# Kernel tuning notes

Hardware: AMD Instinct MI355X
Metric: run time of the kernel (lower is better)

The kernel has to match this reference:

```python
import jax, jax.numpy as jnp
import numpy as np

UNITS = 1024
D_Q = 1024
D_V = 1024


def setup_inputs() -> dict:
    key = jax.random.key(0)
    ks = jax.random.split(key, 8)
    B, S = 32, 2048
    query = jax.random.normal(ks[0], (B, D_Q), dtype=jnp.float32)
    values = jax.random.normal(ks[1], (B, S, D_V), dtype=jnp.float32)
    # Keras Dense params (glorot-ish scale for weights, zero bias init kept random-free)
    W1 = jax.random.normal(ks[2], (D_V, UNITS), dtype=jnp.float32) / np.sqrt(D_V)
    b1 = jnp.zeros((UNITS,), dtype=jnp.float32)
    W2 = jax.random.normal(ks[3], (D_Q, UNITS), dtype=jnp.float32) / np.sqrt(D_Q)
    b2 = jnp.zeros((UNITS,), dtype=jnp.float32)
    V = jax.random.normal(ks[4], (UNITS, 1), dtype=jnp.float32) / np.sqrt(UNITS)
    bV = jnp.zeros((1,), dtype=jnp.float32)
    return {"query": query, "values": values, "W1": W1, "b1": b1,
            "W2": W2, "b2": b2, "V": V, "bV": bV}


def reference(query, values, W1, b1, W2, b2, V, bV):
    # query: [B, d_q], values: [B, S, d_v]
    proj_v = jnp.einsum('bsd,du->bsu', values, W1) + b1        # [B, S, U]
    proj_q = (query @ W2 + b2)[:, None, :]                      # [B, 1, U]
    score = jnp.tanh(proj_v + proj_q) @ V + bV                  # [B, S, 1]
    attention_weights = jax.nn.softmax(score, axis=1)           # [B, S, 1]
    context_vector = jnp.sum(attention_weights * values, axis=1)  # [B, d_v]
    return (context_vector, attention_weights)
```

## Files before the change

### kernel.cpp

```cpp
#include <hip/hip_runtime.h>
#include <math.h>

#define B_  32
#define S_  2048
#define DV  1024
#define U_  1024

typedef __attribute__((ext_vector_type(8))) short bf16x8;
typedef __attribute__((ext_vector_type(4))) float f32x4;

__device__ inline unsigned short f2bf(float f) {
    unsigned int x = __float_as_uint(f);
    return (unsigned short)((x + 0x7fffu + ((x >> 16) & 1u)) >> 16);
}

__device__ inline float tanh_fast(float x) {
    float ax = fabsf(x);
    float e  = __expf(ax + ax);
    float t  = 1.0f - __fdividef(2.0f, e + 1.0f);
    return copysignf(t, x);
}

__device__ __forceinline__ void gload16(const void* g, void* l) {
    __builtin_amdgcn_global_load_lds(
        (const __attribute__((address_space(1))) void*)g,
        (__attribute__((address_space(3))) void*)l,
        16, 0, 0);
}

#define ASM_VMCNT(N) asm volatile("s_waitcnt vmcnt(" #N ")" ::: "memory")
#define ASM_LGKM0()  do { asm volatile("s_waitcnt lgkmcnt(0)" ::: "memory"); \
                          __builtin_amdgcn_sched_barrier(0); } while (0)

__global__ void init_kernel(const float* __restrict__ b1, const float* __restrict__ b2,
                            float* __restrict__ t, float* __restrict__ ctx,
                            float* __restrict__ scores) {
    int i = blockIdx.x * 256 + threadIdx.x;
    scores[i] = 0.f;
    if (i < B_ * U_) {
        int u = i & (U_ - 1);
        t[i]   = b1[u] + b2[u];
        ctx[i] = 0.f;
    }
}

__global__ void projq_kernel(const float* __restrict__ q, const float* __restrict__ W2,
                             float* __restrict__ t) {
    int b  = blockIdx.x;
    int ks = blockIdx.y;
    int tid = threadIdx.x;
    __shared__ float qs[64];
    if (tid < 64) qs[tid] = q[b * DV + ks * 64 + tid];
    __syncthreads();
    float a0 = 0.f, a1 = 0.f, a2 = 0.f, a3 = 0.f;
    const float* w = W2 + (size_t)(ks * 64) * U_;
    for (int d = 0; d < 64; ++d) {
        float qd = qs[d];
        const float* wr = w + (size_t)d * U_ + tid;
        a0 += qd * wr[0];
        a1 += qd * wr[256];
        a2 += qd * wr[512];
        a3 += qd * wr[768];
    }
    atomicAdd(&t[b * U_ + tid      ], a0);
    atomicAdd(&t[b * U_ + tid + 256], a1);
    atomicAdd(&t[b * U_ + tid + 512], a2);
    atomicAdd(&t[b * U_ + tid + 768], a3);
}

__global__ void cvt_values_tiled(const float* __restrict__ v, char* __restrict__ o) {
    size_t t = (size_t)blockIdx.x * 256 + threadIdx.x;
    size_t i = t * 8;
    int row = (int)(i >> 10);
    int k   = (int)(i & 1023);
    float4 f0 = *(const float4*)(v + i);
    float4 f1 = *(const float4*)(v + i + 4);
    union { unsigned short s[8]; uint4 u; } p;
    p.s[0] = f2bf(f0.x); p.s[1] = f2bf(f0.y); p.s[2] = f2bf(f0.z); p.s[3] = f2bf(f0.w);
    p.s[4] = f2bf(f1.x); p.s[5] = f2bf(f1.y); p.s[6] = f2bf(f1.z); p.s[7] = f2bf(f1.w);
    int stile = row >> 8, rt = row & 255, h = rt >> 7, r = rt & 127;
    int kt = k >> 6, kk = k & 63;
    int pchunk = (kk >> 3) ^ (r & 7);
    size_t dst = (size_t)stile * 524288 + (size_t)kt * 32768
               + h * 16384 + r * 128 + pchunk * 16;
    *(uint4*)(o + dst) = p.u;
}

__global__ void prep_w1t(const float* __restrict__ W1, unsigned short* __restrict__ W1T) {
    __shared__ float tile[64][65];
    int k0 = blockIdx.x * 64, u0 = blockIdx.y * 64;
    int t = threadIdx.x;
    int lr = t >> 4, lc = (t & 15) * 4;
#pragma unroll
    for (int i = 0; i < 4; ++i) {
        float4 f = *(const float4*)&W1[(size_t)(k0 + lr + i * 16) * U_ + u0 + lc];
        tile[lr + i * 16][lc + 0] = f.x; tile[lr + i * 16][lc + 1] = f.y;
        tile[lr + i * 16][lc + 2] = f.z; tile[lr + i * 16][lc + 3] = f.w;
    }
    __syncthreads();
    int ur = t >> 2, kq = (t & 3) * 16;
    union { unsigned short s[8]; uint4 u; } p0, p1;
#pragma unroll
    for (int e = 0; e < 8; ++e) p0.s[e] = f2bf(tile[kq + e][ur]);
#pragma unroll
    for (int e = 0; e < 8; ++e) p1.s[e] = f2bf(tile[kq + 8 + e][ur]);
    unsigned short* dst = W1T + (size_t)(u0 + ur) * 1024 + k0 + kq;
    *(uint4*)dst       = p0.u;
    *(uint4*)(dst + 8) = p1.u;
}

#define MFMA16(MB, NB)                                                          \
    _Pragma("unroll") for (int ks = 0; ks < 2; ++ks)                            \
    _Pragma("unroll") for (int n = 0; n < 2; ++n)                               \
    _Pragma("unroll") for (int m = 0; m < 4; ++m)                               \
        acc[(MB)+m][(NB)+n] = __builtin_amdgcn_mfma_f32_16x16x32_bf16(          \
            af[m][ks], bf[n][ks], acc[(MB)+m][(NB)+n], 0, 0, 0);

__launch_bounds__(512, 2)
__global__ void scores_mfma8(const char* __restrict__ AbfT,
                             const unsigned short* __restrict__ W1T,
                             const float* __restrict__ tvec,
                             const float* __restrict__ V,
                             float* __restrict__ scores) {
    __shared__ __align__(16) char lds[131072];

    const int tid  = threadIdx.x;
    const int lane = tid & 63;
    const int wave = tid >> 6;
    const int wm   = wave >> 2;
    const int wn   = wave & 3;
    const int l15  = lane & 15;
    const int lq   = lane >> 4;

    const int id    = blockIdx.x;
    const int wg    = (id & 7) * 128 + (id >> 3);
    const int utile = wg & 3;
    const int stile = wg >> 2;
    const size_t row0 = (size_t)stile * 256;
    const int b       = (int)(row0 >> 11);
    const int s_local = (int)(row0 & 2047);
    const int u0      = utile * 256;

    const char* aBase = AbfT + (size_t)stile * 524288 + wave * 1024 + lane * 16;
    const int rowst = wave * 8 + (lane >> 3);
    const int kch8  = ((lane & 7) ^ ((lane >> 3) & 7)) * 8;
    const unsigned short* bSrc = W1T + (size_t)(u0 + rowst) * 1024 + kch8;
    char* const dstW = lds + wave * 1024;

    const int ao0 = wm * 16384 + l15 * 128 + ((lq ^ (l15 & 7)) << 4);
    const int ao1 = ao0 ^ 64;
    const int bo0 = 32768 + (wn >> 1) * 16384 + (wn & 1) * 8192
                  + l15 * 128 + ((lq ^ (l15 & 7)) << 4);
    const int bo1 = bo0 ^ 64;

    f32x4 acc[8][4];
#pragma unroll
    for (int m = 0; m < 8; ++m)
#pragma unroll
        for (int n = 0; n < 4; ++n) acc[m][n] = (f32x4)0.f;

    bf16x8 af[4][2];
    bf16x8 bf[2][2];

    auto stageA = [&](size_t gOff, int dOff) {
        gload16(aBase + gOff,        dstW + dOff);
        gload16(aBase + gOff + 8192, dstW + dOff + 8192);
    };
    auto stageB = [&](const unsigned short* s, int dOff) {
        gload16(s,             dstW + dOff);
        gload16(s + 64 * 1024, dstW + dOff + 8192);
    };
    auto readA4 = [&](int base) {
#pragma unroll
        for (int m = 0; m < 4; ++m) {
            af[m][0] = *(const bf16x8*)(lds + base + m * 2048 + ao0);
            af[m][1] = *(const bf16x8*)(lds + base + m * 2048 + ao1);
        }
    };
    auto readB2 = [&](int base) {
#pragma unroll
        for (int n = 0; n < 2; ++n) {
            bf[n][0] = *(const bf16x8*)(lds + base + n * 2048 + bo0);
            bf[n][1] = *(const bf16x8*)(lds + base + n * 2048 + bo1);
        }
    };

    stageA(0,     0);
    stageA(16384, 16384);
    stageB(bSrc,          32768);
    stageB(bSrc + 131072, 49152);
    stageA(32768, 65536);
    __builtin_amdgcn_sched_barrier(0);
    ASM_VMCNT(2);
    __builtin_amdgcn_s_barrier();
    __builtin_amdgcn_sched_barrier(0);

    for (int it = 0; it < 8; ++it) {
        const bool pf = (it < 7);
        const size_t aIt = (size_t)it * 65536;
        readA4(0);
        readB2(0);
        stageA(aIt + 49152, 81920);
        __builtin_amdgcn_s_barrier();
        ASM_LGKM0();
        __builtin_amdgcn_s_setprio(1);
        MFMA16(0, 0);
        __builtin_amdgcn_s_setprio(0);
        __builtin_amdgcn_s_barrier();
        readB2(2 * 2048);
        stageB(bSrc + 64, 98304);
        __builtin_amdgcn_s_barrier();
        ASM_LGKM0();
        __builtin_amdgcn_s_setprio(1);
        MFMA16(0, 2);
        __builtin_amdgcn_s_setprio(0);
        __builtin_amdgcn_s_barrier();
        readA4(4 * 2048);
        stageB(bSrc + 64 + 131072, 114688);
        __builtin_amdgcn_s_barrier();
        ASM_LGKM0();
        __builtin_amdgcn_s_setprio(1);
        MFMA16(4, 2);
        __builtin_amdgcn_s_setprio(0);
        __builtin_amdgcn_s_barrier();
        readB2(0);
        if (pf) stageA(aIt + 65536, 0);
        __builtin_amdgcn_s_barrier();
        ASM_LGKM0();
        __builtin_amdgcn_s_setprio(1);
        MFMA16(4, 0);
        __builtin_amdgcn_s_setprio(0);
        __builtin_amdgcn_sched_barrier(0);
        if (pf) { ASM_VMCNT(2); } else { ASM_VMCNT(0); }
        __builtin_amdgcn_s_barrier();
        __builtin_amdgcn_sched_barrier(0);
        readA4(65536);
        readB2(65536);
        if (pf) stageA(aIt + 81920, 16384);
        __builtin_amdgcn_s_barrier();
        ASM_LGKM0();
        __builtin_amdgcn_s_setprio(1);
        MFMA16(0, 0);
        __builtin_amdgcn_s_setprio(0);
        __builtin_amdgcn_s_barrier();
        readB2(65536 + 2 * 2048);
        if (pf) stageB(bSrc + 128, 32768);
        __builtin_amdgcn_s_barrier();
        ASM_LGKM0();
        __builtin_amdgcn_s_setprio(1);
        MFMA16(0, 2);
        __builtin_amdgcn_s_setprio(0);
        __builtin_amdgcn_s_barrier();
        readA4(65536 + 4 * 2048);
        if (pf) stageB(bSrc + 128 + 131072, 49152);
        __builtin_amdgcn_s_barrier();
        ASM_LGKM0();
        __builtin_amdgcn_s_setprio(1);
        MFMA16(4, 2);
        __builtin_amdgcn_s_setprio(0);
        __builtin_amdgcn_s_barrier();
        readB2(65536);
        if (pf) stageA(aIt + 98304, 65536);
        __builtin_amdgcn_s_barrier();
        ASM_LGKM0();
        __builtin_amdgcn_s_setprio(1);
        MFMA16(4, 0);
        __builtin_amdgcn_s_setprio(0);
        __builtin_amdgcn_sched_barrier(0);
        if (pf) { ASM_VMCNT(2); }
        __builtin_amdgcn_s_barrier();
        __builtin_amdgcn_sched_barrier(0);

        bSrc += 128;
    }

    __syncthreads();
    float* fscore = (float*)lds;
    if (tid < 256) fscore[tid] = 0.f;
    __syncthreads();
    float tu[4], vu[4];
#pragma unroll
    for (int n = 0; n < 4; ++n) {
        int u = u0 + wn * 64 + n * 16 + l15;
        tu[n] = tvec[b * U_ + u];
        vu[n] = V[u];
    }
#pragma unroll
    for (int m = 0; m < 8; ++m) {
#pragma unroll
        for (int r = 0; r < 4; ++r) {
            float p = 0.f;
#pragma unroll
            for (int n = 0; n < 4; ++n) p += tanh_fast(acc[m][n][r] + tu[n]) * vu[n];
            p += __shfl_xor(p, 1);
            p += __shfl_xor(p, 2);
            p += __shfl_xor(p, 4);
            p += __shfl_xor(p, 8);
            if (l15 == 0) atomicAdd(&fscore[wm * 128 + m * 16 + lq * 4 + r], p);
        }
    }
    __syncthreads();
    if (tid < 256) atomicAdd(&scores[(size_t)b * S_ + s_local + tid], fscore[tid]);
}

template<bool ABF16>
__launch_bounds__(256, 2)
__global__ void scores_mfma(const void* __restrict__ aPtr,
                            const unsigned short* __restrict__ W1T,
                            const float* __restrict__ t,
                            const float* __restrict__ V,
                            float* __restrict__ scores) {
    __shared__ unsigned short sA[128 * 40];
    __shared__ unsigned short sB[256 * 40];
    __shared__ float fscore[128];

    const int tid  = threadIdx.x;
    const int lane = tid & 63;
    const int wave = tid >> 6;
    const int wm = wave & 1, wn = wave >> 1;
    const int l15 = lane & 15, lq = lane >> 4;

    const int id    = blockIdx.x;
    const int utile = (id >> 3) & 3;
    const int stile = (id & 7) | ((id >> 5) << 3);
    const size_t row0 = (size_t)stile * 128;
    const int b       = (int)(row0 >> 11);
    const int s_local = (int)(row0 & 2047);
    const int u0      = utile * 256;

    if (tid < 128) fscore[tid] = 0.f;

    const int ar = tid >> 1, ak = (tid & 1) << 4;
    const int br = tid >> 1, bk = (tid & 1) << 4;

    const float* Af = (const float*)aPtr + (row0 + ar) * 1024 + ak;
    const unsigned short* Ab = (const unsigned short*)aPtr + (row0 + ar) * 1024 + ak;
    const unsigned short* Bp0 = W1T + (size_t)(u0 + br) * 1024 + bk;
    const unsigned short* Bp1 = Bp0 + 128 * 1024;

    f32x4 acc[4][8];
#pragma unroll
    for (int i = 0; i < 4; ++i)
#pragma unroll
        for (int j = 0; j < 8; ++j) acc[i][j] = (f32x4)0.f;

    uint4 sa0, sa1, sb0, sb1, sb2, sb3;
    float4 fa0, fa1, fa2, fa3;

    if (ABF16) {
        sa0 = *(const uint4*)(Ab);
        sa1 = *(const uint4*)(Ab + 8);
    } else {
        fa0 = *(const float4*)(Af);
        fa1 = *(const float4*)(Af + 4);
        fa2 = *(const float4*)(Af + 8);
        fa3 = *(const float4*)(Af + 12);
    }
    sb0 = *(const uint4*)(Bp0);
    sb1 = *(const uint4*)(Bp0 + 8);
    sb2 = *(const uint4*)(Bp1);
    sb3 = *(const uint4*)(Bp1 + 8);

    for (int k0 = 0; k0 < 1024; k0 += 32) {
        __syncthreads();
        if (ABF16) {
            *(uint4*)&sA[ar * 40 + ak]     = sa0;
            *(uint4*)&sA[ar * 40 + ak + 8] = sa1;
        } else {
            union { unsigned short s[8]; uint4 u; } p0, p1;
            p0.s[0] = f2bf(fa0.x); p0.s[1] = f2bf(fa0.y); p0.s[2] = f2bf(fa0.z); p0.s[3] = f2bf(fa0.w);
            p0.s[4] = f2bf(fa1.x); p0.s[5] = f2bf(fa1.y); p0.s[6] = f2bf(fa1.z); p0.s[7] = f2bf(fa1.w);
            p1.s[0] = f2bf(fa2.x); p1.s[1] = f2bf(fa2.y); p1.s[2] = f2bf(fa2.z); p1.s[3] = f2bf(fa2.w);
            p1.s[4] = f2bf(fa3.x); p1.s[5] = f2bf(fa3.y); p1.s[6] = f2bf(fa3.z); p1.s[7] = f2bf(fa3.w);
            *(uint4*)&sA[ar * 40 + ak]     = p0.u;
            *(uint4*)&sA[ar * 40 + ak + 8] = p1.u;
        }
        *(uint4*)&sB[br * 40 + bk]           = sb0;
        *(uint4*)&sB[br * 40 + bk + 8]       = sb1;
        *(uint4*)&sB[(br + 128) * 40 + bk]     = sb2;
        *(uint4*)&sB[(br + 128) * 40 + bk + 8] = sb3;

        if (k0 + 32 < 1024) {
            int nk = k0 + 32;
            if (ABF16) {
                sa0 = *(const uint4*)(Ab + nk);
                sa1 = *(const uint4*)(Ab + nk + 8);
            } else {
                fa0 = *(const float4*)(Af + nk);
                fa1 = *(const float4*)(Af + nk + 4);
                fa2 = *(const float4*)(Af + nk + 8);
                fa3 = *(const float4*)(Af + nk + 12);
            }
            sb0 = *(const uint4*)(Bp0 + nk);
            sb1 = *(const uint4*)(Bp0 + nk + 8);
            sb2 = *(const uint4*)(Bp1 + nk);
            sb3 = *(const uint4*)(Bp1 + nk + 8);
        }
        __syncthreads();

        bf16x8 af[4];
#pragma unroll
        for (int i = 0; i < 4; ++i)
            af[i] = *(const bf16x8*)&sA[(64 * wm + 16 * i + l15) * 40 + lq * 8];
#pragma unroll
        for (int j = 0; j < 8; ++j) {
            bf16x8 bfj = *(const bf16x8*)&sB[(128 * wn + 16 * j + l15) * 40 + lq * 8];
#pragma unroll
            for (int i = 0; i < 4; ++i)
                acc[i][j] = __builtin_amdgcn_mfma_f32_16x16x32_bf16(af[i], bfj, acc[i][j], 0, 0, 0);
        }
    }

    float tu[8], vu[8];
#pragma unroll
    for (int j = 0; j < 8; ++j) {
        int u = u0 + 128 * wn + 16 * j + l15;
        tu[j] = t[b * U_ + u];
        vu[j] = V[u];
    }
#pragma unroll
    for (int i = 0; i < 4; ++i) {
#pragma unroll
        for (int r = 0; r < 4; ++r) {
            float p = 0.f;
#pragma unroll
            for (int j = 0; j < 8; ++j) p += tanh_fast(acc[i][j][r] + tu[j]) * vu[j];
            p += __shfl_xor(p, 1);
            p += __shfl_xor(p, 2);
            p += __shfl_xor(p, 4);
            p += __shfl_xor(p, 8);
            if (l15 == 0) atomicAdd(&fscore[64 * wm + 16 * i + lq * 4 + r], p);
        }
    }
    __syncthreads();
    if (tid < 128) atomicAdd(&scores[(size_t)b * S_ + s_local + tid], fscore[tid]);
}

__launch_bounds__(256, 2)
__global__ void scores_vec(const float* __restrict__ values, const float* __restrict__ W1,
                           const float* __restrict__ t, const float* __restrict__ V,
                           float* __restrict__ scores) {
    __shared__ float vA[16][132];
    __shared__ float vB[16][68];
    __shared__ float fscore[128];
    const int b   = blockIdx.y;
    const int s0  = blockIdx.x * 128;
    const int tid = threadIdx.x;
    const int tx  = tid & 15, ty = tid >> 4;
    if (tid < 128) fscore[tid] = 0.f;
    const float* vbase = values + ((size_t)b * S_ + s0) * (size_t)DV;
    const int lm = tid >> 2, lkq = (tid & 3) * 4;
    const int lbk = tid >> 4, lbj = (tid & 15) * 4;
    for (int nt = 0; nt < U_ / 64; ++nt) {
        const int u0 = nt * 64;
        float acc[8][4];
#pragma unroll
        for (int i = 0; i < 8; ++i)
#pragma unroll
            for (int j = 0; j < 4; ++j) acc[i][j] = 0.f;
        for (int k0 = 0; k0 < DV; k0 += 16) {
            __syncthreads();
            const float4 v0 = *(const float4*)(vbase + (size_t)lm * DV + k0 + lkq);
            const float4 v1 = *(const float4*)(vbase + (size_t)(lm + 64) * DV + k0 + lkq);
            vA[lkq + 0][lm] = v0.x; vA[lkq + 1][lm] = v0.y;
            vA[lkq + 2][lm] = v0.z; vA[lkq + 3][lm] = v0.w;
            vA[lkq + 0][lm + 64] = v1.x; vA[lkq + 1][lm + 64] = v1.y;
            vA[lkq + 2][lm + 64] = v1.z; vA[lkq + 3][lm + 64] = v1.w;
            *(float4*)&vB[lbk][lbj] = *(const float4*)(W1 + (size_t)(k0 + lbk) * U_ + u0 + lbj);
            __syncthreads();
#pragma unroll
            for (int k = 0; k < 16; ++k) {
                float4 va0 = *(const float4*)&vA[k][ty * 8];
                float4 va1 = *(const float4*)&vA[k][ty * 8 + 4];
                float4 vb  = *(const float4*)&vB[k][tx * 4];
                float a_[8] = {va0.x, va0.y, va0.z, va0.w, va1.x, va1.y, va1.z, va1.w};
                float b_[4] = {vb.x, vb.y, vb.z, vb.w};
#pragma unroll
                for (int i = 0; i < 8; ++i)
#pragma unroll
                    for (int j = 0; j < 4; ++j) acc[i][j] += a_[i] * b_[j];
            }
        }
        float tq[4], vv[4];
#pragma unroll
        for (int j = 0; j < 4; ++j) {
            int u = u0 + tx * 4 + j;
            tq[j] = t[b * U_ + u];
            vv[j] = V[u];
        }
#pragma unroll
        for (int i = 0; i < 8; ++i) {
            float p = 0.f;
#pragma unroll
            for (int j = 0; j < 4; ++j) p += tanhf(acc[i][j] + tq[j]) * vv[j];
            p += __shfl_down(p, 8, 16);
            p += __shfl_down(p, 4, 16);
            p += __shfl_down(p, 2, 16);
            p += __shfl_down(p, 1, 16);
            if (tx == 0) fscore[ty * 8 + i] += p;
        }
    }
    __syncthreads();
    if (tid < 128) scores[(size_t)b * S_ + s0 + tid] = fscore[tid];
}

__global__ void softmax_kernel(const float* __restrict__ scores, float* __restrict__ wout) {
    int b = blockIdx.x;
    int tid = threadIdx.x;
    __shared__ float red[256];
    float v[8];
    float m = -1e30f;
#pragma unroll
    for (int i = 0; i < 8; ++i) {
        v[i] = scores[(size_t)b * S_ + tid + i * 256];
        m = fmaxf(m, v[i]);
    }
    red[tid] = m; __syncthreads();
    for (int off = 128; off > 0; off >>= 1) {
        if (tid < off) red[tid] = fmaxf(red[tid], red[tid + off]);
        __syncthreads();
    }
    m = red[0];
    __syncthreads();
    float s = 0.f;
#pragma unroll
    for (int i = 0; i < 8; ++i) { v[i] = __expf(v[i] - m); s += v[i]; }
    red[tid] = s; __syncthreads();
    for (int off = 128; off > 0; off >>= 1) {
        if (tid < off) red[tid] += red[tid + off];
        __syncthreads();
    }
    float inv = 1.f / red[0];
#pragma unroll
    for (int i = 0; i < 8; ++i) wout[(size_t)b * S_ + tid + i * 256] = v[i] * inv;
}

__global__ void context_kernel(const float* __restrict__ values, const float* __restrict__ w,
                               float* __restrict__ ctx) {
    int b   = blockIdx.x;
    int sc  = blockIdx.y;
    int tid = threadIdx.x;
    __shared__ float ws_[128];
    if (tid < 128) ws_[tid] = w[(size_t)b * S_ + sc * 128 + tid];
    __syncthreads();
    const float4* vp = (const float4*)(values + ((size_t)b * S_ + sc * 128) * DV) + tid;
    float ax = 0.f, ay = 0.f, az = 0.f, aw = 0.f;
#pragma unroll 4
    for (int s = 0; s < 128; ++s) {
        float4 v = vp[(size_t)s * 256];
        float wv = ws_[s];
        ax += wv * v.x; ay += wv * v.y; az += wv * v.z; aw += wv * v.w;
    }
    float* c = ctx + b * DV + tid * 4;
    atomicAdd(c + 0, ax); atomicAdd(c + 1, ay);
    atomicAdd(c + 2, az); atomicAdd(c + 3, aw);
}

extern "C" void kernel_launch(void* const* d_in, const int* in_sizes, int n_in,
                              void* d_out, int out_size, void* d_ws, size_t ws_size,
                              hipStream_t stream) {
    const float* query  = (const float*)d_in[0];
    const float* values = (const float*)d_in[1];
    const float* W1     = (const float*)d_in[2];
    const float* b1     = (const float*)d_in[3];
    const float* W2     = (const float*)d_in[4];
    const float* b2     = (const float*)d_in[5];
    const float* V      = (const float*)d_in[6];

    float* out  = (float*)d_out;
    float* ctx  = out;
    float* wout = out + B_ * DV;

    char* ws = (char*)d_ws;
    const size_t W1T_BYTES = (size_t)U_ * DV * 2;
    const size_t T_BYTES   = (size_t)B_ * U_ * 4;
    const size_t SC_BYTES  = (size_t)B_ * S_ * 4;
    const size_t ABF_BYTES = (size_t)B_ * S_ * DV * 2;

    if (ws_size >= W1T_BYTES + T_BYTES + SC_BYTES + ABF_BYTES) {
        unsigned short* W1T = (unsigned short*)ws;
        float* t      = (float*)(ws + W1T_BYTES);
        float* scores = t + B_ * U_;
        char*  AbfT   = (char*)(scores + B_ * S_);

        init_kernel     <<<dim3(256),      256, 0, stream>>>(b1, b2, t, ctx, scores);
        projq_kernel    <<<dim3(32, 16),   256, 0, stream>>>(query, W2, t);
        cvt_values_tiled<<<dim3(32768),    256, 0, stream>>>(values, AbfT);
        prep_w1t        <<<dim3(16, 16),   256, 0, stream>>>(W1, W1T);
        scores_mfma8    <<<dim3(1024),     512, 0, stream>>>(AbfT, W1T, t, V, scores);
        softmax_kernel  <<<dim3(32),       256, 0, stream>>>(scores, wout);
        context_kernel  <<<dim3(32, 16),   256, 0, stream>>>(values, wout, ctx);
    } else if (ws_size >= W1T_BYTES + T_BYTES + SC_BYTES) {
        unsigned short* W1T = (unsigned short*)ws;
        float* t      = (float*)(ws + W1T_BYTES);
        float* scores = t + B_ * U_;

        init_kernel   <<<dim3(256),      256, 0, stream>>>(b1, b2, t, ctx, scores);
        projq_kernel  <<<dim3(32, 16),   256, 0, stream>>>(query, W2, t);
        prep_w1t      <<<dim3(16, 16),   256, 0, stream>>>(W1, W1T);
        scores_mfma<false><<<dim3(2048), 256, 0, stream>>>(values, W1T, t, V, scores);
        softmax_kernel<<<dim3(32),       256, 0, stream>>>(scores, wout);
        context_kernel<<<dim3(32, 16),   256, 0, stream>>>(values, wout, ctx);
    } else {
        float* t      = (float*)ws;
        float* scores = t + B_ * U_;

        init_kernel   <<<dim3(256),      256, 0, stream>>>(b1, b2, t, ctx, scores);
        projq_kernel  <<<dim3(32, 16),   256, 0, stream>>>(query, W2, t);
        scores_vec    <<<dim3(16, 32),   256, 0, stream>>>(values, W1, t, V, scores);
        softmax_kernel<<<dim3(32),       256, 0, stream>>>(scores, wout);
        context_kernel<<<dim3(32, 16),   256, 0, stream>>>(values, wout, ctx);
    }
}
```

Measured before the change: 603.9 us.

## Fuse prep kernels into one launch and merge softmax with context

Merges init, query projection, values bf16 conversion and W1 transpose into a single heterogeneous kernel that picks its role from the block index. The query projection now has each block do a full-K dot product, so it writes the bias-plus-projection result directly without atomics. Softmax and the context reduction are fused into one kernel in which every block recomputes the row max and sum for its batch before weighting its 128-row slice. This cuts the launch count from seven to three and removes inter-kernel gaps, at the cost of redundant softmax reductions across the 16 slices of each batch row.

New measurement: 616.1 us. +2.0%, slower.

```diff
diff --git a/kernel.cpp b/kernel.cpp
--- a/kernel.cpp
+++ b/kernel.cpp
@@ -31,6 +31,330 @@
 #define ASM_VMCNT(N) asm volatile("s_waitcnt vmcnt(" #N ")" ::: "memory")
 #define ASM_LGKM0()  do { asm volatile("s_waitcnt lgkmcnt(0)" ::: "memory"); \
                           __builtin_amdgcn_sched_barrier(0); } while (0)
+
+__global__ __launch_bounds__(256)
+void fused_prep(const float* __restrict__ values, char* __restrict__ AbfT,
+                const float* __restrict__ W1, unsigned short* __restrict__ W1T,
+                const float* __restrict__ query, const float* __restrict__ W2,
+                const float* __restrict__ b1, const float* __restrict__ b2,
+                float* __restrict__ t, float* __restrict__ scores,
+                float* __restrict__ ctx) {
+    const int bid = blockIdx.x;
+    const int tid = threadIdx.x;
+
+    if (bid < 32768) {
+        size_t i = ((size_t)bid * 256 + tid) * 8;
+        int row = (int)(i >> 10);
+        int k   = (int)(i & 1023);
+        float4 f0 = *(const float4*)(values + i);
+        float4 f1 = *(const float4*)(values + i + 4);
+        union { unsigned short s[8]; uint4 u; } p;
+        p.s[0] = f2bf(f0.x); p.s[1] = f2bf(f0.y); p.s[2] = f2bf(f0.z); p.s[3] = f2bf(f0.w);
+        p.s[4] = f2bf(f1.x); p.s[5] = f2bf(f1.y); p.s[6] = f2bf(f1.z); p.s[7] = f2bf(f1.w);
+        int stile = row >> 8, rt = row & 255, h = rt >> 7, r = rt & 127;
+        int kt = k >> 6, kk = k & 63;
+        int pchunk = (kk >> 3) ^ (r & 7);
+        size_t dst = (size_t)stile * 524288 + (size_t)kt * 32768
+                   + h * 16384 + r * 128 + pchunk * 16;
+        *(uint4*)(AbfT + dst) = p.u;
+    } else if (bid < 33024) {
+        __shared__ float tile[64][65];
+        int i = bid - 32768;
+        int k0 = (i & 15) * 64, u0 = (i >> 4) * 64;
+        int lr = tid >> 4, lc = (tid & 15) * 4;
+#pragma unroll
+        for (int j = 0; j < 4; ++j) {
+            float4 f = *(const float4*)&W1[(size_t)(k0 + lr + j * 16) * U_ + u0 + lc];
+            tile[lr + j * 16][lc + 0] = f.x; tile[lr + j * 16][lc + 1] = f.y;
+            tile[lr + j * 16][lc + 2] = f.z; tile[lr + j * 16][lc + 3] = f.w;
+        }
+        __syncthreads();
+        int ur = tid >> 2, kq = (tid & 3) * 16;
+        union { unsigned short s[8]; uint4 u; } p0, p1;
+#pragma unroll
+        for (int e = 0; e < 8; ++e) p0.s[e] = f2bf(tile[kq + e][ur]);
+#pragma unroll
+        for (int e = 0; e < 8; ++e) p1.s[e] = f2bf(tile[kq + 8 + e][ur]);
+        unsigned short* dst = W1T + (size_t)(u0 + ur) * 1024 + k0 + kq;
+        *(uint4*)dst       = p0.u;
+        *(uint4*)(dst + 8) = p1.u;
+    } else if (bid < 33152) {
+        __shared__ float qs2[1024];
+        int i = bid - 33024;
+        int b = i >> 2, uq = i & 3;
+        for (int j = tid; j < 1024; j += 256) qs2[j] = query[b * DV + j];
+        __syncthreads();
+        int u = uq * 256 + tid;
+        float a0 = 0.f, a1 = 0.f, a2 = 0.f, a3 = 0.f;
+        float a4 = 0.f, a5 = 0.f, a6 = 0.f, a7 = 0.f;
+        const float* w = W2 + u;
+        for (int k = 0; k < 1024; k += 8) {
+            a0 += qs2[k + 0] * w[(size_t)(k + 0) * U_];
+            a1 += qs2[k + 1] * w[(size_t)(k + 1) * U_];
+            a2 += qs2[k + 2] * w[(size_t)(k + 2) * U_];
+            a3 += qs2[k + 3] * w[(size_t)(k + 3) * U_];
+            a4 += qs2[k + 4] * w[(size_t)(k + 4) * U_];
+            a5 += qs2[k + 5] * w[(size_t)(k + 5) * U_];
+            a6 += qs2[k + 6] * w[(size_t)(k + 6) * U_];
+            a7 += qs2[k + 7] * w[(size_t)(k + 7) * U_];
+        }
+        t[b * U_ + u] = b1[u] + b2[u]
+                      + ((a0 + a1) + (a2 + a3)) + ((a4 + a5) + (a6 + a7));
+    } else if (bid < 33408) {
+        scores[(bid - 33152) * 256 + tid] = 0.f;
+    } else {
+        ctx[(bid - 33408) * 256 + tid] = 0.f;
+    }
+}
+
+#define MFMA16(MB, NB)                                                          \
+    _Pragma("unroll") for (int ks = 0; ks < 2; ++ks)                            \
+    _Pragma("unroll") for (int n = 0; n < 2; ++n)                               \
+    _Pragma("unroll") for (int m = 0; m < 4; ++m)                               \
+        acc[(MB)+m][(NB)+n] = __builtin_amdgcn_mfma_f32_16x16x32_bf16(          \
+            af[m][ks], bf[n][ks], acc[(MB)+m][(NB)+n], 0, 0, 0);
+
+__launch_bounds__(512, 2)
+__global__ void scores_mfma8(const char* __restrict__ AbfT,
+                             const unsigned short* __restrict__ W1T,
+                             const float* __restrict__ tvec,
+                             const float* __restrict__ V,
+                             float* __restrict__ scores) {
+    __shared__ __align__(16) char lds[131072];
+
+    const int tid  = threadIdx.x;
+    const int lane = tid & 63;
+    const int wave = tid >> 6;
+    const int wm   = wave >> 2;
+    const int wn   = wave & 3;
+    const int l15  = lane & 15;
+    const int lq   = lane >> 4;
+
+    const int id    = blockIdx.x;
+    const int wg    = (id & 7) * 128 + (id >> 3);
+    const int utile = wg & 3;
+    const int stile = wg >> 2;
+    const size_t row0 = (size_t)stile * 256;
+    const int b       = (int)(row0 >> 11);
+    const int s_local = (int)(row0 & 2047);
+    const int u0      = utile * 256;
+
+    const char* aBase = AbfT + (size_t)stile * 524288 + wave * 1024 + lane * 16;
+    const int rowst = wave * 8 + (lane >> 3);
+    const int kch8  = ((lane & 7) ^ ((lane >> 3) & 7)) * 8;
+    const unsigned short* bSrc = W1T + (size_t)(u0 + rowst) * 1024 + kch8;
+    char* const dstW = lds + wave * 1024;
+
+    const int ao0 = wm * 16384 + l15 * 128 + ((lq ^ (l15 & 7)) << 4);
+    const int ao1 = ao0 ^ 64;
+    const int bo0 = 32768 + (wn >> 1) * 16384 + (wn & 1) * 8192
+                  + l15 * 128 + ((lq ^ (l15 & 7)) << 4);
+    const int bo1 = bo0 ^ 64;
+
+    f32x4 acc[8][4];
+#pragma unroll
+    for (int m = 0; m < 8; ++m)
+#pragma unroll
+        for (int n = 0; n < 4; ++n) acc[m][n] = (f32x4)0.f;
+
+    bf16x8 af[4][2];
+    bf16x8 bf[2][2];
+
+    auto stageA = [&](size_t gOff, int dOff) {
+        gload16(aBase + gOff,        dstW + dOff);
+        gload16(aBase + gOff + 8192, dstW + dOff + 8192);
+    };
+    auto stageB = [&](const unsigned short* s, int dOff) {
+        gload16(s,             dstW + dOff);
+        gload16(s + 64 * 1024, dstW + dOff + 8192);
+    };
+    auto readA4 = [&](int base) {
+#pragma unroll
+        for (int m = 0; m < 4; ++m) {
+            af[m][0] = *(const bf16x8*)(lds + base + m * 2048 + ao0);
+            af[m][1] = *(const bf16x8*)(lds + base + m * 2048 + ao1);
+        }
+    };
+    auto readB2 = [&](int base) {
+#pragma unroll
+        for (int n = 0; n < 2; ++n) {
+            bf[n][0] = *(const bf16x8*)(lds + base + n * 2048 + bo0);
+            bf[n][1] = *(const bf16x8*)(lds + base + n * 2048 + bo1);
+        }
+    };
+
+    stageA(0,     0);
+    stageA(16384, 16384);
+    stageB(bSrc,          32768);
+    stageB(bSrc + 131072, 49152);
+    stageA(32768, 65536);
+    __builtin_amdgcn_sched_barrier(0);
+    ASM_VMCNT(2);
+    __builtin_amdgcn_s_barrier();
+    __builtin_amdgcn_sched_barrier(0);
+
+    for (int it = 0; it < 8; ++it) {
+        const bool pf = (it < 7);
+        const size_t aIt = (size_t)it * 65536;
+        readA4(0);
+        readB2(0);
+        stageA(aIt + 49152, 81920);
+        __builtin_amdgcn_s_barrier();
+        ASM_LGKM0();
+        __builtin_amdgcn_s_setprio(1);
+        MFMA16(0, 0);
+        __builtin_amdgcn_s_setprio(0);
+        __builtin_amdgcn_s_barrier();
+        readB2(2 * 2048);
+        stageB(bSrc + 64, 98304);
+        __builtin_amdgcn_s_barrier();
+        ASM_LGKM0();
+        __builtin_amdgcn_s_setprio(1);
+        MFMA16(0, 2);
+        __builtin_amdgcn_s_setprio(0);
+        __builtin_amdgcn_s_barrier();
+        readA4(4 * 2048);
+        stageB(bSrc + 64 + 131072, 114688);
+        __builtin_amdgcn_s_barrier();
+        ASM_LGKM0();
+        __builtin_amdgcn_s_setprio(1);
+        MFMA16(4, 2);
+        __builtin_amdgcn_s_setprio(0);
+        __builtin_amdgcn_s_barrier();
+        readB2(0);
+        if (pf) stageA(aIt + 65536, 0);
+        __builtin_amdgcn_s_barrier();
+        ASM_LGKM0();
+        __builtin_amdgcn_s_setprio(1);
+        MFMA16(4, 0);
+        __builtin_amdgcn_s_setprio(0);
+        __builtin_amdgcn_sched_barrier(0);
+        if (pf) { ASM_VMCNT(2); } else { ASM_VMCNT(0); }
+        __builtin_amdgcn_s_barrier();
+        __builtin_amdgcn_sched_barrier(0);
+        readA4(65536);
+        readB2(65536);
+        if (pf) stageA(aIt + 81920, 16384);
+        __builtin_amdgcn_s_barrier();
+        ASM_LGKM0();
+        __builtin_amdgcn_s_setprio(1);
+        MFMA16(0, 0);
+        __builtin_amdgcn_s_setprio(0);
+        __builtin_amdgcn_s_barrier();
+        readB2(65536 + 2 * 2048);
+        if (pf) stageB(bSrc + 128, 32768);
+        __builtin_amdgcn_s_barrier();
+        ASM_LGKM0();
+        __builtin_amdgcn_s_setprio(1);
+        MFMA16(0, 2);
+        __builtin_amdgcn_s_setprio(0);
+        __builtin_amdgcn_s_barrier();
+        readA4(65536 + 4 * 2048);
+        if (pf) stageB(bSrc + 128 + 131072, 49152);
+        __builtin_amdgcn_s_barrier();
+        ASM_LGKM0();
+        __builtin_amdgcn_s_setprio(1);
+        MFMA16(4, 2);
+        __builtin_amdgcn_s_setprio(0);
+        __builtin_amdgcn_s_barrier();
+        readB2(65536);
+        if (pf) stageA(aIt + 98304, 65536);
+        __builtin_amdgcn_s_barrier();
+        ASM_LGKM0();
+        __builtin_amdgcn_s_setprio(1);
+        MFMA16(4, 0);
+        __builtin_amdgcn_s_setprio(0);
+        __builtin_amdgcn_sched_barrier(0);
+        if (pf) { ASM_VMCNT(2); }
+        __builtin_amdgcn_s_barrier();
+        __builtin_amdgcn_sched_barrier(0);
+
+        bSrc += 128;
+    }
+
+    __syncthreads();
+    float* fscore = (float*)lds;
+    if (tid < 256) fscore[tid] = 0.f;
+    __syncthreads();
+    float tu[4], vu[4];
+#pragma unroll
+    for (int n = 0; n < 4; ++n) {
+        int u = u0 + wn * 64 + n * 16 + l15;
+        tu[n] = tvec[b * U_ + u];
+        vu[n] = V[u];
+    }
+#pragma unroll
+    for (int m = 0; m < 8; ++m) {
+#pragma unroll
+        for (int r = 0; r < 4; ++r) {
+            float p = 0.f;
+#pragma unroll
+            for (int n = 0; n < 4; ++n) p += tanh_fast(acc[m][n][r] + tu[n]) * vu[n];
+            p += __shfl_xor(p, 1);
+            p += __shfl_xor(p, 2);
+            p += __shfl_xor(p, 4);
+            p += __shfl_xor(p, 8);
+            if (l15 == 0) atomicAdd(&fscore[wm * 128 + m * 16 + lq * 4 + r], p);
+        }
+    }
+    __syncthreads();
+    if (tid < 256) atomicAdd(&scores[(size_t)b * S_ + s_local + tid], fscore[tid]);
+}
+
+__global__ __launch_bounds__(256)
+void fused_sm_ctx(const float* __restrict__ scores, const float* __restrict__ values,
+                  float* __restrict__ wout, float* __restrict__ ctx) {
+    const int b   = blockIdx.x;
+    const int sc  = blockIdx.y;
+    const int tid = threadIdx.x;
+    __shared__ float red[256];
+    __shared__ float ws_[128];
+
+    float v[8];
+    float m = -1e30f;
+#pragma unroll
+    for (int i = 0; i < 8; ++i) {
+        v[i] = scores[(size_t)b * S_ + tid + i * 256];
+        m = fmaxf(m, v[i]);
+    }
+    red[tid] = m; __syncthreads();
+    for (int off = 128; off > 0; off >>= 1) {
+        if (tid < off) red[tid] = fmaxf(red[tid], red[tid + off]);
+        __syncthreads();
+    }
+    m = red[0];
+    __syncthreads();
+    float s = 0.f;
+#pragma unroll
+    for (int i = 0; i < 8; ++i) s += __expf(v[i] - m);
+    red[tid] = s; __syncthreads();
+    for (int off = 128; off > 0; off >>= 1) {
+        if (tid < off) red[tid] += red[tid + off];
+        __syncthreads();
+    }
+    float inv = 1.f / red[0];
+    __syncthreads();
+
+    if (tid < 128) {
+        float x = scores[(size_t)b * S_ + sc * 128 + tid];
+        float w = __expf(x - m) * inv;
+        ws_[tid] = w;
+        wout[(size_t)b * S_ + sc * 128 + tid] = w;
+    }
+    __syncthreads();
+
+    const float4* vp = (const float4*)(values + ((size_t)b * S_ + sc * 128) * DV) + tid;
+    float ax = 0.f, ay = 0.f, az = 0.f, aw = 0.f;
+#pragma unroll 4
+    for (int s2 = 0; s2 < 128; ++s2) {
+        float4 vv = vp[(size_t)s2 * 256];
+        float wv = ws_[s2];
+        ax += wv * vv.x; ay += wv * vv.y; az += wv * vv.z; aw += wv * vv.w;
+    }
+    float* c = ctx + b * DV + tid * 4;
+    atomicAdd(c + 0, ax); atomicAdd(c + 1, ay);
+    atomicAdd(c + 2, az); atomicAdd(c + 3, aw);
+}
 
 __global__ void init_kernel(const float* __restrict__ b1, const float* __restrict__ b2,
                             float* __restrict__ t, float* __restrict__ ctx,
@@ -68,24 +392,6 @@
     atomicAdd(&t[b * U_ + tid + 768], a3);
 }
 
-__global__ void cvt_values_tiled(const float* __restrict__ v, char* __restrict__ o) {
-    size_t t = (size_t)blockIdx.x * 256 + threadIdx.x;
-    size_t i = t * 8;
-    int row = (int)(i >> 10);
-    int k   = (int)(i & 1023);
-    float4 f0 = *(const float4*)(v + i);
-    float4 f1 = *(const float4*)(v + i + 4);
-    union { unsigned short s[8]; uint4 u; } p;
-    p.s[0] = f2bf(f0.x); p.s[1] = f2bf(f0.y); p.s[2] = f2bf(f0.z); p.s[3] = f2bf(f0.w);
-    p.s[4] = f2bf(f1.x); p.s[5] = f2bf(f1.y); p.s[6] = f2bf(f1.z); p.s[7] = f2bf(f1.w);
-    int stile = row >> 8, rt = row & 255, h = rt >> 7, r = rt & 127;
-    int kt = k >> 6, kk = k & 63;
-    int pchunk = (kk >> 3) ^ (r & 7);
-    size_t dst = (size_t)stile * 524288 + (size_t)kt * 32768
-               + h * 16384 + r * 128 + pchunk * 16;
-    *(uint4*)(o + dst) = p.u;
-}
-
 __global__ void prep_w1t(const float* __restrict__ W1, unsigned short* __restrict__ W1T) {
     __shared__ float tile[64][65];
     int k0 = blockIdx.x * 64, u0 = blockIdx.y * 64;
@@ -107,200 +413,6 @@
     unsigned short* dst = W1T + (size_t)(u0 + ur) * 1024 + k0 + kq;
     *(uint4*)dst       = p0.u;
     *(uint4*)(dst + 8) = p1.u;
-}
-
-#define MFMA16(MB, NB)                                                          \
-    _Pragma("unroll") for (int ks = 0; ks < 2; ++ks)                            \
-    _Pragma("unroll") for (int n = 0; n < 2; ++n)                               \
-    _Pragma("unroll") for (int m = 0; m < 4; ++m)                               \
-        acc[(MB)+m][(NB)+n] = __builtin_amdgcn_mfma_f32_16x16x32_bf16(          \
-            af[m][ks], bf[n][ks], acc[(MB)+m][(NB)+n], 0, 0, 0);
-
-__launch_bounds__(512, 2)
-__global__ void scores_mfma8(const char* __restrict__ AbfT,
-                             const unsigned short* __restrict__ W1T,
-                             const float* __restrict__ tvec,
-                             const float* __restrict__ V,
-                             float* __restrict__ scores) {
-    __shared__ __align__(16) char lds[131072];
-
-    const int tid  = threadIdx.x;
-    const int lane = tid & 63;
-    const int wave = tid >> 6;
-    const int wm   = wave >> 2;
-    const int wn   = wave & 3;
-    const int l15  = lane & 15;
-    const int lq   = lane >> 4;
-
-    const int id    = blockIdx.x;
-    const int wg    = (id & 7) * 128 + (id >> 3);
-    const int utile = wg & 3;
-    const int stile = wg >> 2;
-    const size_t row0 = (size_t)stile * 256;
-    const int b       = (int)(row0 >> 11);
-    const int s_local = (int)(row0 & 2047);
-    const int u0      = utile * 256;
-
-    const char* aBase = AbfT + (size_t)stile * 524288 + wave * 1024 + lane * 16;
-    const int rowst = wave * 8 + (lane >> 3);
-    const int kch8  = ((lane & 7) ^ ((lane >> 3) & 7)) * 8;
-    const unsigned short* bSrc = W1T + (size_t)(u0 + rowst) * 1024 + kch8;
-    char* const dstW = lds + wave * 1024;
-
-    const int ao0 = wm * 16384 + l15 * 128 + ((lq ^ (l15 & 7)) << 4);
-    const int ao1 = ao0 ^ 64;
-    const int bo0 = 32768 + (wn >> 1) * 16384 + (wn & 1) * 8192
-                  + l15 * 128 + ((lq ^ (l15 & 7)) << 4);
-    const int bo1 = bo0 ^ 64;
-
-    f32x4 acc[8][4];
-#pragma unroll
-    for (int m = 0; m < 8; ++m)
-#pragma unroll
-        for (int n = 0; n < 4; ++n) acc[m][n] = (f32x4)0.f;
-
-    bf16x8 af[4][2];
-    bf16x8 bf[2][2];
-
-    auto stageA = [&](size_t gOff, int dOff) {
-        gload16(aBase + gOff,        dstW + dOff);
-        gload16(aBase + gOff + 8192, dstW + dOff + 8192);
-    };
-    auto stageB = [&](const unsigned short* s, int dOff) {
-        gload16(s,             dstW + dOff);
-        gload16(s + 64 * 1024, dstW + dOff + 8192);
-    };
-    auto readA4 = [&](int base) {
-#pragma unroll
-        for (int m = 0; m < 4; ++m) {
-            af[m][0] = *(const bf16x8*)(lds + base + m * 2048 + ao0);
-            af[m][1] = *(const bf16x8*)(lds + base + m * 2048 + ao1);
-        }
-    };
-    auto readB2 = [&](int base) {
-#pragma unroll
-        for (int n = 0; n < 2; ++n) {
-            bf[n][0] = *(const bf16x8*)(lds + base + n * 2048 + bo0);
-            bf[n][1] = *(const bf16x8*)(lds + base + n * 2048 + bo1);
-        }
-    };
-
-    stageA(0,     0);
-    stageA(16384, 16384);
-    stageB(bSrc,          32768);
-    stageB(bSrc + 131072, 49152);
-    stageA(32768, 65536);
-    __builtin_amdgcn_sched_barrier(0);
-    ASM_VMCNT(2);
-    __builtin_amdgcn_s_barrier();
-    __builtin_amdgcn_sched_barrier(0);
-
-    for (int it = 0; it < 8; ++it) {
-        const bool pf = (it < 7);
-        const size_t aIt = (size_t)it * 65536;
-        readA4(0);
-        readB2(0);
-        stageA(aIt + 49152, 81920);
-        __builtin_amdgcn_s_barrier();
-        ASM_LGKM0();
-        __builtin_amdgcn_s_setprio(1);
-        MFMA16(0, 0);
-        __builtin_amdgcn_s_setprio(0);
-        __builtin_amdgcn_s_barrier();
-        readB2(2 * 2048);
-        stageB(bSrc + 64, 98304);
-        __builtin_amdgcn_s_barrier();
-        ASM_LGKM0();
-        __builtin_amdgcn_s_setprio(1);
-        MFMA16(0, 2);
-        __builtin_amdgcn_s_setprio(0);
-        __builtin_amdgcn_s_barrier();
-        readA4(4 * 2048);
-        stageB(bSrc + 64 + 131072, 114688);
-        __builtin_amdgcn_s_barrier();
-        ASM_LGKM0();
-        __builtin_amdgcn_s_setprio(1);
-        MFMA16(4, 2);
-        __builtin_amdgcn_s_setprio(0);
-        __builtin_amdgcn_s_barrier();
-        readB2(0);
-        if (pf) stageA(aIt + 65536, 0);
-        __builtin_amdgcn_s_barrier();
-        ASM_LGKM0();
-        __builtin_amdgcn_s_setprio(1);
-        MFMA16(4, 0);
-        __builtin_amdgcn_s_setprio(0);
-        __builtin_amdgcn_sched_barrier(0);
-        if (pf) { ASM_VMCNT(2); } else { ASM_VMCNT(0); }
-        __builtin_amdgcn_s_barrier();
-        __builtin_amdgcn_sched_barrier(0);
-        readA4(65536);
-        readB2(65536);
-        if (pf) stageA(aIt + 81920, 16384);
-        __builtin_amdgcn_s_barrier();
-        ASM_LGKM0();
-        __builtin_amdgcn_s_setprio(1);
-        MFMA16(0, 0);
-        __builtin_amdgcn_s_setprio(0);
-        __builtin_amdgcn_s_barrier();
-        readB2(65536 + 2 * 2048);
-        if (pf) stageB(bSrc + 128, 32768);
-        __builtin_amdgcn_s_barrier();
-        ASM_LGKM0();
-        __builtin_amdgcn_s_setprio(1);
-        MFMA16(0, 2);
-        __builtin_amdgcn_s_setprio(0);
-        __builtin_amdgcn_s_barrier();
-        readA4(65536 + 4 * 2048);
-        if (pf) stageB(bSrc + 128 + 131072, 49152);
-        __builtin_amdgcn_s_barrier();
-        ASM_LGKM0();
-        __builtin_amdgcn_s_setprio(1);
-        MFMA16(4, 2);
-        __builtin_amdgcn_s_setprio(0);
-        __builtin_amdgcn_s_barrier();
-        readB2(65536);
-        if (pf) stageA(aIt + 98304, 65536);
-        __builtin_amdgcn_s_barrier();
-        ASM_LGKM0();
-        __builtin_amdgcn_s_setprio(1);
-        MFMA16(4, 0);
-        __builtin_amdgcn_s_setprio(0);
-        __builtin_amdgcn_sched_barrier(0);
-        if (pf) { ASM_VMCNT(2); }
-        __builtin_amdgcn_s_barrier();
-        __builtin_amdgcn_sched_barrier(0);
-
-        bSrc += 128;
-    }
-
-    __syncthreads();
-    float* fscore = (float*)lds;
-    if (tid < 256) fscore[tid] = 0.f;
-    __syncthreads();
-    float tu[4], vu[4];
-#pragma unroll
-    for (int n = 0; n < 4; ++n) {
-        int u = u0 + wn * 64 + n * 16 + l15;
-        tu[n] = tvec[b * U_ + u];
-        vu[n] = V[u];
-    }
-#pragma unroll
-    for (int m = 0; m < 8; ++m) {
-#pragma unroll
-        for (int r = 0; r < 4; ++r) {
-            float p = 0.f;
-#pragma unroll
-            for (int n = 0; n < 4; ++n) p += tanh_fast(acc[m][n][r] + tu[n]) * vu[n];
-            p += __shfl_xor(p, 1);
-            p += __shfl_xor(p, 2);
-            p += __shfl_xor(p, 4);
-            p += __shfl_xor(p, 8);
-            if (l15 == 0) atomicAdd(&fscore[wm * 128 + m * 16 + lq * 4 + r], p);
-        }
-    }
-    __syncthreads();
-    if (tid < 256) atomicAdd(&scores[(size_t)b * S_ + s_local + tid], fscore[tid]);
 }
 
 template<bool ABF16>
@@ -583,13 +695,11 @@
         float* scores = t + B_ * U_;
         char*  AbfT   = (char*)(scores + B_ * S_);
 
-        init_kernel     <<<dim3(256),      256, 0, stream>>>(b1, b2, t, ctx, scores);
-        projq_kernel    <<<dim3(32, 16),   256, 0, stream>>>(query, W2, t);
-        cvt_values_tiled<<<dim3(32768),    256, 0, stream>>>(values, AbfT);
-        prep_w1t        <<<dim3(16, 16),   256, 0, stream>>>(W1, W1T);
-        scores_mfma8    <<<dim3(1024),     512, 0, stream>>>(AbfT, W1T, t, V, scores);
-        softmax_kernel  <<<dim3(32),       256, 0, stream>>>(scores, wout);
-        context_kernel  <<<dim3(32, 16),   256, 0, stream>>>(values, wout, ctx);
+        fused_prep  <<<dim3(33536),   256, 0, stream>>>(values, AbfT, W1, W1T,
+                                                        query, W2, b1, b2,
+                                                        t, scores, ctx);
+        scores_mfma8<<<dim3(1024),    512, 0, stream>>>(AbfT, W1T, t, V, scores);
+        fused_sm_ctx<<<dim3(32, 16),  256, 0, stream>>>(scores, values, wout, ctx);
     } else if (ws_size >= W1T_BYTES + T_BYTES + SC_BYTES) {
         unsigned short* W1T = (unsigned short*)ws;
         float* t      = (float*)(ws + W1T_BYTES);
```
